# Optimization experiments

Measured on AMD Instinct MI355X. Metric: run time of the kernel, lower is better.

Reference implementation:

```python
import jax, jax.numpy as jnp
import numpy as np
from jax import lax

B, CIN, COUT, H, W = 8, 256, 256, 96, 96


def _conv_bn(x, w, g, b, act):
    # 3x3 conv, stride 1, SAME padding (NCHW / OIHW), then per-channel affine (folded BN)
    y = lax.conv_general_dilated(x, w, (1, 1), 'SAME',
                                 dimension_numbers=('NCHW', 'OIHW', 'NCHW'))
    y = y * g[None, :, None, None] + b[None, :, None, None]
    return jax.nn.relu(y) if act else y


def setup_inputs() -> dict:
    key = jax.random.key(0)
    ks = jax.random.split(key, 16)
    def wgt(k, cout, cin):
        return jax.random.normal(k, (cout, cin, 3, 3), jnp.float32) * (1.0 / np.sqrt(cin * 9))
    def gb(k, c):
        k1, k2 = jax.random.split(k)
        return (1.0 + 0.1 * jax.random.normal(k1, (c,), jnp.float32),
                0.1 * jax.random.normal(k2, (c,), jnp.float32))
    g_p1, b_p1 = gb(ks[1], COUT); g_p2, b_p2 = gb(ks[3], COUT)
    g_p, b_p = gb(ks[5], COUT); g_c1, b_c1 = gb(ks[7], COUT); g_c2, b_c2 = gb(ks[9], COUT)
    return {
        'x': jax.random.normal(ks[0], (B, CIN, H, W), jnp.float32),
        'w_p1': wgt(ks[10], COUT, CIN), 'g_p1': g_p1, 'b_p1': b_p1,
        'w_p2': wgt(ks[11], COUT, CIN), 'g_p2': g_p2, 'b_p2': b_p2,
        'w_p': wgt(ks[12], COUT, COUT), 'g_p': g_p, 'b_p': b_p,
        'w_c1': wgt(ks[13], COUT, CIN), 'g_c1': g_c1, 'b_c1': b_c1,
        'w_c2': wgt(ks[14], COUT, COUT), 'g_c2': g_c2, 'b_c2': b_c2,
    }


def reference(x, w_p1, g_p1, b_p1, w_p2, g_p2, b_p2, w_p, g_p, b_p,
              w_c1, g_c1, b_c1, w_c2, g_c2, b_c2):
    # branch 1: conv -> TopPool (cummax up, i.e. reverse along H) -> BottomPool (cummax down)
    p1 = _conv_bn(x, w_p1, g_p1, b_p1, act=True)
    pool1 = lax.cummax(p1, axis=2, reverse=True)   # TopPool
    pool1 = lax.cummax(pool1, axis=2)              # BottomPool
    # branch 2: conv -> LeftPool (reverse along W) -> RightPool
    p2 = _conv_bn(x, w_p2, g_p2, b_p2, act=True)
    pool2 = lax.cummax(p2, axis=3, reverse=True)   # LeftPool
    pool2 = lax.cummax(pool2, axis=3)              # RightPool
    p_conv = _conv_bn(pool1 + pool2, w_p, g_p, b_p, act=False)
    conv1 = _conv_bn(x, w_c1, g_c1, b_c1, act=False)
    relu = jax.nn.relu(p_conv + conv1)
    return _conv_bn(relu, w_c2, g_c2, b_c2, act=True)
```

## Files before the change

### kernel.cpp

```cpp
#include <hip/hip_runtime.h>


typedef _Float16 f16x8 __attribute__((ext_vector_type(8)));
typedef _Float16 f16x4v __attribute__((ext_vector_type(4)));
typedef float f32x4 __attribute__((ext_vector_type(4)));

#define HP 98
#define WP 98
#define KTOT 2304
#define WSET (256*KTOT)
#define XPAD_E ((size_t)8*HP*WP*256)
#define UVP_E  ((size_t)8*98*256)
#define UV2_E  ((size_t)3*8*96*256)
#define WUV_SET 196608

__device__ __forceinline__ int xcd_swz(int bid, int nwg)
{
  return (bid & 7) * (nwg >> 3) + (bid >> 3);
}

#define BUF_Q 24576
#define SMEM_Q 49152

struct CtxQ {
  unsigned goff[6];
  unsigned mask;
  unsigned lds_stage;
  unsigned aoff;
  int wl, quad, wv;
  int b, h0, w0;
};

template<int SW>
__device__ __forceinline__ CtxQ make_ctxQ(int spatial, int ch)
{
  CtxQ c;
  c.b = spatial / 36;
  const int tt = spatial - c.b * 36;
  const int ht = tt / 6, wt = tt - ht * 6;
  c.h0 = ht * 16; c.w0 = wt * 16;
  const int tid = threadIdx.x, lane = tid & 63;
  c.wv = tid >> 6;
  c.quad = lane >> 4; c.wl = lane & 15;
  c.aoff = (unsigned)((ch * 4 + c.wv * 2) * 512 + c.wl * 32 + c.quad * 8);
  const unsigned base_hw = (unsigned)(c.b * HP + c.h0) * WP + c.w0;
  const int lg = lane >> 2;
  c.mask = 0;
#pragma unroll
  for (int t = 0; t < 6; ++t) {
    const int s = (c.wv * 12 + t) * 16 + lg;
    const int x = s / 18, y = s - x * 18;
    const int wh = SW ? y : x, ww = SW ? x : y;
    c.goff[t] = (base_hw + (unsigned)(wh * WP + ww)) * 256u + (lane & 3) * 8u;
    if (y >= 12) c.mask |= (1u << t);
    if (s > 227) c.mask |= (1u << (6 + t));
  }
  c.lds_stage = (unsigned)(c.wv * 12) * 1024u + (unsigned)lane * 16u;
  return c;
}

template<int SW>
__device__ __forceinline__ void stage_cbQ(const _Float16* __restrict__ src,
                                          char* sbuf, const CtxQ& c, int buf, int cb)
{
  constexpr int D0 = SW ? (6 * WP + 5) * 256 : (5 * WP + 6) * 256;
  constexpr int D1 = SW ? (6 - 12 * WP) * 256 : (6 * WP - 12) * 256;
  char* l0 = sbuf + buf * BUF_Q + c.lds_stage;
#pragma unroll
  for (int t = 0; t < 6; ++t) {
    const _Float16* g = src + c.goff[t] + cb * 32;
    __builtin_amdgcn_global_load_lds(
        (const __attribute__((address_space(1))) void*)g,
        (__attribute__((address_space(3))) void*)(l0 + t * 1024), 16, 0, 0);
  }
#pragma unroll
  for (int t = 0; t < 6; ++t) {
    const int d = ((c.mask >> (6 + t)) & 1) ? 0
                : (((c.mask >> t) & 1) ? D1 : D0);
    const _Float16* g = src + (int)(c.goff[t] + (unsigned)d) + cb * 32;
    __builtin_amdgcn_global_load_lds(
        (const __attribute__((address_space(1))) void*)g,
        (__attribute__((address_space(3))) void*)(l0 + (6 + t) * 1024), 16, 0, 0);
  }
}

template<int S>
__device__ __forceinline__ void conv_accumQ(const _Float16* __restrict__ src,
                                            const _Float16* __restrict__ wkb,
                                            char* sbuf, const CtxQ& c, f32x4 acc[2][16])
{
  const _Float16* A0 = wkb + c.aoff;
  stage_cbQ<S>(src, sbuf, c, 0, 0);
#pragma unroll 1
  for (int cb = 0; cb < 8; ++cb) {
    __syncthreads();
    if (cb < 7) stage_cbQ<S>(src, sbuf, c, (cb + 1) & 1, cb + 1);
    const _Float16* B = (const _Float16*)(sbuf + (cb & 1) * BUF_Q);
    const _Float16* A = A0 + cb * (9 * 8192);
#pragma unroll
    for (int o = 0; o < 3; ++o) {
      f16x8 af[3][2];
#pragma unroll
      for (int p = 0; p < 3; ++p) {
        const int tap = (S == 0) ? p * 3 + o : o * 3 + p;
#pragma unroll
        for (int i = 0; i < 2; ++i)
          af[p][i] = *(const f16x8*)(A + tap * 8192 + i * 512);
      }
#pragma unroll
      for (int jh = 0; jh < 2; ++jh) {
        f16x8 cache[10];
#pragma unroll
        for (int r = 0; r < 10; ++r)
          cache[r] = *(const f16x8*)(B + ((jh * 8 + r) * 18 + c.wl + o) * 32 + c.quad * 8);
#pragma unroll
        for (int p = 0; p < 3; ++p)
#pragma unroll
          for (int i = 0; i < 2; ++i)
#pragma unroll
            for (int j = 0; j < 8; ++j)
              acc[i][jh * 8 + j] = __builtin_amdgcn_mfma_f32_16x16x32_f16(
                  af[p][i], cache[j + p], acc[i][jh * 8 + j], 0, 0, 0);
      }
    }
  }
  __syncthreads();
}

#define ZERO_ACCQ(acc) \
  _Pragma("unroll") for (int i = 0; i < 2; ++i) \
  _Pragma("unroll") for (int j = 0; j < 16; ++j) acc[i][j] = (f32x4){0.f,0.f,0.f,0.f};

__global__ __launch_bounds__(128, 2) void k_conv_p12(
    const _Float16* __restrict__ xpad, const _Float16* __restrict__ wk,
    const float* __restrict__ bias1, const float* __restrict__ bias2,
    float* __restrict__ u_pad, float* __restrict__ v_pad)
{
  __shared__ __align__(16) char smem[SMEM_Q];
  const int lin = xcd_swz(blockIdx.x, 2304);
  const int set = lin >= 1152;
  const int rem = lin - set * 1152;
  const int spatial = rem >> 2, ch = rem & 3;
  f32x4 acc[2][16];
  ZERO_ACCQ(acc)
  if (set == 0) {
    CtxQ c = make_ctxQ<0>(spatial, ch);
    conv_accumQ<0>(xpad, wk, smem, c, acc);
#pragma unroll
    for (int i = 0; i < 2; ++i) {
      const int co = (ch * 4 + c.wv * 2 + i) * 16 + c.quad * 4;
      const float4 bs = *(const float4*)(bias1 + co);
      float m0 = 0.f, m1 = 0.f, m2 = 0.f, m3 = 0.f;
#pragma unroll
      for (int j = 0; j < 16; ++j) {
        m0 = fmaxf(m0, acc[i][j][0] + bs.x);
        m1 = fmaxf(m1, acc[i][j][1] + bs.y);
        m2 = fmaxf(m2, acc[i][j][2] + bs.z);
        m3 = fmaxf(m3, acc[i][j][3] + bs.w);
      }
      unsigned* tgt = (unsigned*)(u_pad + ((size_t)c.b * 98 + (c.w0 + c.wl + 1)) * 256 + co);
      atomicMax(tgt + 0, __float_as_uint(m0));
      atomicMax(tgt + 1, __float_as_uint(m1));
      atomicMax(tgt + 2, __float_as_uint(m2));
      atomicMax(tgt + 3, __float_as_uint(m3));
    }
  } else {
    CtxQ c = make_ctxQ<1>(spatial, ch);
    conv_accumQ<1>(xpad, wk + WSET, smem, c, acc);
#pragma unroll
    for (int i = 0; i < 2; ++i) {
      const int co = (ch * 4 + c.wv * 2 + i) * 16 + c.quad * 4;
      const float4 bs = *(const float4*)(bias2 + co);
      float m0 = 0.f, m1 = 0.f, m2 = 0.f, m3 = 0.f;
#pragma unroll
      for (int j = 0; j < 16; ++j) {
        m0 = fmaxf(m0, acc[i][j][0] + bs.x);
        m1 = fmaxf(m1, acc[i][j][1] + bs.y);
        m2 = fmaxf(m2, acc[i][j][2] + bs.z);
        m3 = fmaxf(m3, acc[i][j][3] + bs.w);
      }
      unsigned* tgt = (unsigned*)(v_pad + ((size_t)c.b * 98 + (c.h0 + c.wl + 1)) * 256 + co);
      atomicMax(tgt + 0, __float_as_uint(m0));
      atomicMax(tgt + 1, __float_as_uint(m1));
      atomicMax(tgt + 2, __float_as_uint(m2));
      atomicMax(tgt + 3, __float_as_uint(m3));
    }
  }
}

__global__ __launch_bounds__(256, 2) void k_uv1d(
    const float* __restrict__ u_pad, const float* __restrict__ v_pad,
    const _Float16* __restrict__ wuv, float* __restrict__ u2, float* __restrict__ v2)
{
  const int id = blockIdx.x;
  const int py = blockIdx.y;
  const int b = id & 7, cs = (id >> 3) % 3, t = id / 24;
  const float* src = t ? v_pad : u_pad;
  float* dst = t ? v2 : u2;
  const _Float16* A0 = wuv + (size_t)(t * 3 + cs) * WUV_SET;
  const int lane = threadIdx.x & 63, wv = threadIdx.x >> 6;
  const int quad = lane >> 4, l16 = lane & 15;

  f32x4 acc[4][3];
#pragma unroll
  for (int i = 0; i < 4; ++i)
#pragma unroll
    for (int j = 0; j < 3; ++j) acc[i][j] = (f32x4){0.f, 0.f, 0.f, 0.f};

#pragma unroll 1
  for (int kb = 0; kb < 24; ++kb) {
    const int dw = kb >> 3, cb = kb & 7;
    f16x8 bf[3];
#pragma unroll
    for (int j = 0; j < 3; ++j) {
      const int pos = py * 48 + j * 16 + l16;
      const float* p = src + ((size_t)b * 98 + (pos + dw)) * 256 + cb * 32 + quad * 8;
      const float4 x0 = *(const float4*)p;
      const float4 x1 = *(const float4*)(p + 4);
      f16x8 v;
      v[0] = (_Float16)x0.x; v[1] = (_Float16)x0.y; v[2] = (_Float16)x0.z; v[3] = (_Float16)x0.w;
      v[4] = (_Float16)x1.x; v[5] = (_Float16)x1.y; v[6] = (_Float16)x1.z; v[7] = (_Float16)x1.w;
      bf[j] = v;
    }
    f16x8 af[4];
#pragma unroll
    for (int i = 0; i < 4; ++i)
      af[i] = *(const f16x8*)(A0 + (size_t)(kb * 16 + wv * 4 + i) * 512 + l16 * 32 + quad * 8);
#pragma unroll
    for (int i = 0; i < 4; ++i)
#pragma unroll
      for (int j = 0; j < 3; ++j)
        acc[i][j] = __builtin_amdgcn_mfma_f32_16x16x32_f16(af[i], bf[j], acc[i][j], 0, 0, 0);
  }
#pragma unroll
  for (int i = 0; i < 4; ++i)
#pragma unroll
    for (int j = 0; j < 3; ++j) {
      const int pos = py * 48 + j * 16 + l16;
      const int co = wv * 64 + i * 16 + quad * 4;
      *(f32x4*)(dst + ((size_t)(cs * 8 + b) * 96 + pos) * 256 + co) = acc[i][j];
    }
}

__global__ __launch_bounds__(128, 2) void k_conv_c1f(
    const _Float16* __restrict__ xpad, const _Float16* __restrict__ wkc1,
    const float* __restrict__ bias_p, const float* __restrict__ bias_c1,
    const float* __restrict__ u2, const float* __restrict__ v2,
    _Float16* __restrict__ rpad)
{
  __shared__ __align__(16) char smem[SMEM_Q];
  const int lin = xcd_swz(blockIdx.x, 1152);
  const int spatial = lin >> 2, ch = lin & 3;
  CtxQ c = make_ctxQ<0>(spatial, ch);
  f32x4 acc[2][16];
  ZERO_ACCQ(acc)
  conv_accumQ<0>(xpad, wkc1, smem, c, acc);

  const int w = c.w0 + c.wl;
  const int wcase = (w == 0) ? 0 : ((w == 95) ? 2 : 1);
#pragma unroll
  for (int i = 0; i < 2; ++i) {
    const int co = (ch * 4 + c.wv * 2 + i) * 16 + c.quad * 4;
    float4 bs = *(const float4*)(bias_p + co);
    const float4 b2 = *(const float4*)(bias_c1 + co);
    bs.x += b2.x; bs.y += b2.y; bs.z += b2.z; bs.w += b2.w;
#pragma unroll
    for (int j = 0; j < 16; ++j) {
      const int h = c.h0 + j;
      const int hcase = (h == 0) ? 0 : ((h == 95) ? 2 : 1);
      const float4 uq = *(const float4*)(u2 + ((size_t)(hcase * 8 + c.b) * 96 + w) * 256 + co);
      const float4 vq = *(const float4*)(v2 + ((size_t)(wcase * 8 + c.b) * 96 + h) * 256 + co);
      f16x4v pk;
      pk[0] = (_Float16)fmaxf(acc[i][j][0] + bs.x + uq.x + vq.x, 0.f);
      pk[1] = (_Float16)fmaxf(acc[i][j][1] + bs.y + uq.y + vq.y, 0.f);
      pk[2] = (_Float16)fmaxf(acc[i][j][2] + bs.z + uq.z + vq.z, 0.f);
      pk[3] = (_Float16)fmaxf(acc[i][j][3] + bs.w + uq.w + vq.w, 0.f);
      *(f16x4v*)(rpad + ((size_t)(c.b * HP + h + 1) * WP + w + 1) * 256 + co) = pk;
    }
  }
}

__global__ __launch_bounds__(128, 2) void k_conv_c2(
    const _Float16* __restrict__ rpad, const _Float16* __restrict__ wkc2,
    const float* __restrict__ bias, float* __restrict__ dout)
{
  __shared__ __align__(16) char smem[SMEM_Q];
  const int lin = xcd_swz(blockIdx.x, 1152);
  const int spatial = lin >> 2, ch = lin & 3;
  CtxQ c = make_ctxQ<0>(spatial, ch);
  f32x4 acc[2][16];
  ZERO_ACCQ(acc)
  conv_accumQ<0>(rpad, wkc2, smem, c, acc);

  const int w = c.w0 + c.wl;
#pragma unroll
  for (int j = 0; j < 16; ++j) {
    const int h = c.h0 + j;
    float* op = dout + (size_t)c.b * 2359296 + h * 96 + w;
#pragma unroll
    for (int i = 0; i < 2; ++i) {
      const int co = (ch * 4 + c.wv * 2 + i) * 16 + c.quad * 4;
      const float4 bs = *(const float4*)(bias + co);
      op[(size_t)(co + 0) * 9216] = fmaxf(acc[i][j][0] + bs.x, 0.f);
      op[(size_t)(co + 1) * 9216] = fmaxf(acc[i][j][1] + bs.y, 0.f);
      op[(size_t)(co + 2) * 9216] = fmaxf(acc[i][j][2] + bs.z, 0.f);
      op[(size_t)(co + 3) * 9216] = fmaxf(acc[i][j][3] + bs.w, 0.f);
    }
  }
}

__global__ void k_border(_Float16* __restrict__ xpad, _Float16* __restrict__ rpad)
{
  const int idx = blockIdx.x, b = blockIdx.y;
  _Float16* buf = blockIdx.z ? rpad : xpad;
  int h, w;
  if (idx < 98)       { h = 0;  w = idx; }
  else if (idx < 196) { h = 97; w = idx - 98; }
  else { const int r = idx - 196; h = 1 + (r >> 1); w = (r & 1) ? 97 : 0; }
  buf[((size_t)(b * HP + h) * WP + w) * 256 + threadIdx.x] = (_Float16)0.f;
}

__global__ void k_pack_x(const float* __restrict__ x, _Float16* __restrict__ xpad)
{
  __shared__ float tile[32][33];
  const int bh = blockIdx.x;
  const int b = bh / 96, h = bh - b * 96;
  const int c0 = blockIdx.y * 32, w0 = blockIdx.z * 32;
  const int tx = threadIdx.x & 31, ty = threadIdx.x >> 5;
#pragma unroll
  for (int i = 0; i < 4; ++i) {
    int cI = c0 + ty + i * 8;
    tile[ty + i * 8][tx] = x[(((size_t)b * 256 + cI) * 96 + h) * 96 + w0 + tx];
  }
  __syncthreads();
#pragma unroll
  for (int i = 0; i < 4; ++i) {
    int w = w0 + ty + i * 8;
    xpad[((size_t)(b * HP + h + 1) * WP + (w + 1)) * 256 + c0 + tx] =
        (_Float16)tile[tx][ty + i * 8];
  }
}

__global__ void k_repack_w(const float* w0, const float* g0, const float* w1, const float* g1,
                           const float* w2, const float* g2, const float* w3, const float* g3,
                           const float* w4, const float* g4, _Float16* __restrict__ wk)
{
  const int set = blockIdx.y;
  const float* w; const float* g;
  switch (set) {
    case 0: w = w0; g = g0; break;
    case 1: w = w1; g = g1; break;
    case 2: w = w2; g = g2; break;
    case 3: w = w3; g = g3; break;
    default: w = w4; g = g4; break;
  }
  const int t = blockIdx.x * 256 + threadIdx.x;
  const int co = t >> 8, ci = t & 255;
  const int cb = ci >> 5, kk = ci & 31, cog = co >> 4, m = co & 15;
  const float gv = g[co];
  const float* src = w + ((size_t)co * 256 + ci) * 9;
  _Float16* dst = wk + (size_t)set * WSET + cog * 512 + m * 32 + kk;
#pragma unroll
  for (int tap = 0; tap < 9; ++tap)
    dst[(cb * 9 + tap) * 8192] = (_Float16)(src[tap] * gv);
}

__global__ void k_repack_uvw(const float* __restrict__ wp, const float* __restrict__ gp,
                             _Float16* __restrict__ wuv)
{
  const int tcs = blockIdx.y;
  const int tt = tcs / 3, cs = tcs - tt * 3;
  const int idx = blockIdx.x * 256 + threadIdx.x;
  const int co = idx >> 8, ci = idx & 255;
  const float gv = gp[co];
  const float* src = wp + ((size_t)co * 256 + ci) * 9;
  const int lo = (cs == 0) ? 1 : 0, hi = (cs == 2) ? 1 : 2;
  _Float16* base = wuv + (size_t)tcs * WUV_SET;
#pragma unroll
  for (int d = 0; d < 3; ++d) {
    float s = 0.f;
    for (int e = lo; e <= hi; ++e)
      s += (tt == 0) ? src[e * 3 + d] : src[d * 3 + e];
    const int k = d * 256 + ci;
    const int kb = k >> 5, kk = k & 31;
    base[(size_t)(kb * 16 + (co >> 4)) * 512 + (co & 15) * 32 + kk] = (_Float16)(s * gv);
  }
}

extern "C" void kernel_launch(void* const* d_in, const int* in_sizes, int n_in,
                              void* d_out, int out_size, void* d_ws, size_t ws_size,
                              hipStream_t stream)
{
  const float* x    = (const float*)d_in[0];
  const float* w_p1 = (const float*)d_in[1];
  const float* g_p1 = (const float*)d_in[2];
  const float* b_p1 = (const float*)d_in[3];
  const float* w_p2 = (const float*)d_in[4];
  const float* g_p2 = (const float*)d_in[5];
  const float* b_p2 = (const float*)d_in[6];
  const float* w_p  = (const float*)d_in[7];
  const float* g_p  = (const float*)d_in[8];
  const float* b_p  = (const float*)d_in[9];
  const float* w_c1 = (const float*)d_in[10];
  const float* g_c1 = (const float*)d_in[11];
  const float* b_c1 = (const float*)d_in[12];
  const float* w_c2 = (const float*)d_in[13];
  const float* g_c2 = (const float*)d_in[14];
  const float* b_c2 = (const float*)d_in[15];

  char* ws = (char*)d_ws;
  size_t off = 0;
  _Float16* x_pad = (_Float16*)(ws + off); off += XPAD_E * 2;
  _Float16* r_pad = (_Float16*)(ws + off); off += XPAD_E * 2;
  _Float16* wks   = (_Float16*)(ws + off); off += (size_t)5 * WSET * 2;
  _Float16* wuv   = (_Float16*)(ws + off); off += (size_t)6 * WUV_SET * 2;
  float*    u_pad = (float*)(ws + off);    off += UVP_E * 4;
  float*    v_pad = (float*)(ws + off);    off += UVP_E * 4;
  float*    u2    = (float*)(ws + off);    off += UV2_E * 4;
  float*    v2    = (float*)(ws + off);    off += UV2_E * 4;
  (void)ws_size; (void)in_sizes; (void)n_in; (void)out_size;

  hipMemsetAsync(u_pad, 0, UVP_E * 4, stream);
  hipMemsetAsync(v_pad, 0, UVP_E * 4, stream);

  k_border    <<<dim3(388, 8, 2), 256, 0, stream>>>(x_pad, r_pad);
  k_pack_x    <<<dim3(768, 8, 3), 256, 0, stream>>>(x, x_pad);
  k_repack_w  <<<dim3(256, 5),    256, 0, stream>>>(w_p1, g_p1, w_p2, g_p2, w_p, g_p,
                                                    w_c1, g_c1, w_c2, g_c2, wks);
  k_repack_uvw<<<dim3(256, 6),    256, 0, stream>>>(w_p, g_p, wuv);
  k_conv_p12  <<<2304, 128, 0, stream>>>(x_pad, wks, b_p1, b_p2, u_pad, v_pad);
  k_uv1d      <<<dim3(48, 2), 256, 0, stream>>>(u_pad, v_pad, wuv, u2, v2);
  k_conv_c1f  <<<1152, 128, 0, stream>>>(x_pad, wks + (size_t)3 * WSET, b_p, b_c1,
                                         u2, v2, r_pad);
  k_conv_c2   <<<1152, 128, 0, stream>>>(r_pad, wks + (size_t)4 * WSET, b_c2,
                                         (float*)d_out);
}
```

Before: 549.9 us.

## Merge conv_c1 into the p1/p2 conv launch and split its epilogue out

The x-sourced c1 convolution moves into the same launch as the p1/p2 convolutions. Blocks grow to 256 threads (four waves, eight 16-channel groups per block), so each staged input tile is reused across twice as many output channels, and staging becomes one 6-load pass per wave. The c1 result is written as fp16 into the output buffer as scratch. A new elementwise kernel then adds u2/v2, applies relu and writes r_pad. This puts more work in one big launch and halves input staging per output channel, but adds an fp16 round trip for the intermediate and an extra kernel.

Result: faster. 522.0 us (-5.1%).

```diff
diff --git a/kernel.cpp b/kernel.cpp
--- a/kernel.cpp
+++ b/kernel.cpp
@@ -24,6 +24,99 @@
 
 struct CtxQ {
   unsigned goff[6];
+  unsigned lds_stage;
+  unsigned aoff;
+  int wl, quad, wv;
+  int b, h0, w0;
+};
+
+template<int SW>
+__device__ __forceinline__ CtxQ make_ctxQ(int spatial, int ch)
+{
+  CtxQ c;
+  c.b = spatial / 36;
+  const int tt = spatial - c.b * 36;
+  const int ht = tt / 6, wt = tt - ht * 6;
+  c.h0 = ht * 16; c.w0 = wt * 16;
+  const int tid = threadIdx.x, lane = tid & 63;
+  c.wv = tid >> 6;
+  c.quad = lane >> 4; c.wl = lane & 15;
+  c.aoff = (unsigned)((ch * 8 + c.wv * 2) * 512 + c.wl * 32 + c.quad * 8);
+  const unsigned base_hw = (unsigned)(c.b * HP + c.h0) * WP + c.w0;
+#pragma unroll
+  for (int t = 0; t < 6; ++t) {
+    int s = (c.wv * 6 + t) * 16 + (lane >> 2);
+    if (s > 323) s = 323;
+    const int x = s / 18, y = s - x * 18;
+    const int wh = SW ? y : x, ww = SW ? x : y;
+    c.goff[t] = (base_hw + (unsigned)(wh * WP + ww)) * 256u + (lane & 3) * 8u;
+  }
+  c.lds_stage = (unsigned)(c.wv * 6) * 1024u + (unsigned)lane * 16u;
+  return c;
+}
+
+__device__ __forceinline__ void stage_cbQ(const _Float16* __restrict__ src,
+                                          char* sbuf, const CtxQ& c, int buf, int cb)
+{
+  char* l0 = sbuf + buf * BUF_Q + c.lds_stage;
+#pragma unroll
+  for (int t = 0; t < 6; ++t) {
+    const _Float16* g = src + c.goff[t] + cb * 32;
+    __builtin_amdgcn_global_load_lds(
+        (const __attribute__((address_space(1))) void*)g,
+        (__attribute__((address_space(3))) void*)(l0 + t * 1024), 16, 0, 0);
+  }
+}
+
+template<int S>
+__device__ __forceinline__ void conv_accumQ(const _Float16* __restrict__ src,
+                                            const _Float16* __restrict__ wkb,
+                                            char* sbuf, const CtxQ& c, f32x4 acc[2][16])
+{
+  const _Float16* A0 = wkb + c.aoff;
+  stage_cbQ(src, sbuf, c, 0, 0);
+#pragma unroll 1
+  for (int cb = 0; cb < 8; ++cb) {
+    __syncthreads();
+    if (cb < 7) stage_cbQ(src, sbuf, c, (cb + 1) & 1, cb + 1);
+    const _Float16* B = (const _Float16*)(sbuf + (cb & 1) * BUF_Q);
+    const _Float16* A = A0 + cb * (9 * 8192);
+#pragma unroll
+    for (int o = 0; o < 3; ++o) {
+      f16x8 af[3][2];
+#pragma unroll
+      for (int p = 0; p < 3; ++p) {
+        const int tap = (S == 0) ? p * 3 + o : o * 3 + p;
+#pragma unroll
+        for (int i = 0; i < 2; ++i)
+          af[p][i] = *(const f16x8*)(A + tap * 8192 + i * 512);
+      }
+#pragma unroll
+      for (int jh = 0; jh < 2; ++jh) {
+        f16x8 cache[10];
+#pragma unroll
+        for (int r = 0; r < 10; ++r)
+          cache[r] = *(const f16x8*)(B + ((jh * 8 + r) * 18 + c.wl + o) * 32 + c.quad * 8);
+#pragma unroll
+        for (int p = 0; p < 3; ++p)
+#pragma unroll
+          for (int i = 0; i < 2; ++i)
+#pragma unroll
+            for (int j = 0; j < 8; ++j)
+              acc[i][jh * 8 + j] = __builtin_amdgcn_mfma_f32_16x16x32_f16(
+                  af[p][i], cache[j + p], acc[i][jh * 8 + j], 0, 0, 0);
+      }
+    }
+  }
+  __syncthreads();
+}
+
+#define ZERO_ACCQ(acc) \
+  _Pragma("unroll") for (int i = 0; i < 2; ++i) \
+  _Pragma("unroll") for (int j = 0; j < 16; ++j) acc[i][j] = (f32x4){0.f,0.f,0.f,0.f};
+
+struct CtxB {
+  unsigned goff[6];
   unsigned mask;
   unsigned lds_stage;
   unsigned aoff;
@@ -32,9 +125,9 @@
 };
 
 template<int SW>
-__device__ __forceinline__ CtxQ make_ctxQ(int spatial, int ch)
-{
-  CtxQ c;
+__device__ __forceinline__ CtxB make_ctxB(int spatial, int ch)
+{
+  CtxB c;
   c.b = spatial / 36;
   const int tt = spatial - c.b * 36;
   const int ht = tt / 6, wt = tt - ht * 6;
@@ -60,8 +153,8 @@
 }
 
 template<int SW>
-__device__ __forceinline__ void stage_cbQ(const _Float16* __restrict__ src,
-                                          char* sbuf, const CtxQ& c, int buf, int cb)
+__device__ __forceinline__ void stage_cbB(const _Float16* __restrict__ src,
+                                          char* sbuf, const CtxB& c, int buf, int cb)
 {
   constexpr int D0 = SW ? (6 * WP + 5) * 256 : (5 * WP + 6) * 256;
   constexpr int D1 = SW ? (6 - 12 * WP) * 256 : (6 * WP - 12) * 256;
@@ -85,16 +178,16 @@
 }
 
 template<int S>
-__device__ __forceinline__ void conv_accumQ(const _Float16* __restrict__ src,
+__device__ __forceinline__ void conv_accumB(const _Float16* __restrict__ src,
                                             const _Float16* __restrict__ wkb,
-                                            char* sbuf, const CtxQ& c, f32x4 acc[2][16])
+                                            char* sbuf, const CtxB& c, f32x4 acc[2][16])
 {
   const _Float16* A0 = wkb + c.aoff;
-  stage_cbQ<S>(src, sbuf, c, 0, 0);
+  stage_cbB<S>(src, sbuf, c, 0, 0);
 #pragma unroll 1
   for (int cb = 0; cb < 8; ++cb) {
     __syncthreads();
-    if (cb < 7) stage_cbQ<S>(src, sbuf, c, (cb + 1) & 1, cb + 1);
+    if (cb < 7) stage_cbB<S>(src, sbuf, c, (cb + 1) & 1, cb + 1);
     const _Float16* B = (const _Float16*)(sbuf + (cb & 1) * BUF_Q);
     const _Float16* A = A0 + cb * (9 * 8192);
 #pragma unroll
@@ -127,63 +220,86 @@
   __syncthreads();
 }
 
-#define ZERO_ACCQ(acc) \
-  _Pragma("unroll") for (int i = 0; i < 2; ++i) \
-  _Pragma("unroll") for (int j = 0; j < 16; ++j) acc[i][j] = (f32x4){0.f,0.f,0.f,0.f};
-
-__global__ __launch_bounds__(128, 2) void k_conv_p12(
+__global__ __launch_bounds__(256, 2) void k_conv_main(
     const _Float16* __restrict__ xpad, const _Float16* __restrict__ wk,
     const float* __restrict__ bias1, const float* __restrict__ bias2,
-    float* __restrict__ u_pad, float* __restrict__ v_pad)
+    const float* __restrict__ bias_p, const float* __restrict__ bias_c1,
+    float* __restrict__ u_pad, float* __restrict__ v_pad,
+    _Float16* __restrict__ tmp)
 {
   __shared__ __align__(16) char smem[SMEM_Q];
-  const int lin = xcd_swz(blockIdx.x, 2304);
-  const int set = lin >= 1152;
-  const int rem = lin - set * 1152;
-  const int spatial = rem >> 2, ch = rem & 3;
+  const int lin = xcd_swz(blockIdx.x, 1728);
   f32x4 acc[2][16];
   ZERO_ACCQ(acc)
-  if (set == 0) {
+  if (lin < 1152) {
+    const int set = lin >= 576;
+    const int rem = lin - set * 576;
+    const int spatial = rem >> 1, ch = rem & 1;
+    if (set == 0) {
+      CtxQ c = make_ctxQ<0>(spatial, ch);
+      conv_accumQ<0>(xpad, wk, smem, c, acc);
+#pragma unroll
+      for (int i = 0; i < 2; ++i) {
+        const int co = (ch * 8 + c.wv * 2 + i) * 16 + c.quad * 4;
+        const float4 bs = *(const float4*)(bias1 + co);
+        float m0 = 0.f, m1 = 0.f, m2 = 0.f, m3 = 0.f;
+#pragma unroll
+        for (int j = 0; j < 16; ++j) {
+          m0 = fmaxf(m0, acc[i][j][0] + bs.x);
+          m1 = fmaxf(m1, acc[i][j][1] + bs.y);
+          m2 = fmaxf(m2, acc[i][j][2] + bs.z);
+          m3 = fmaxf(m3, acc[i][j][3] + bs.w);
+        }
+        unsigned* tgt = (unsigned*)(u_pad + ((size_t)c.b * 98 + (c.w0 + c.wl + 1)) * 256 + co);
+        atomicMax(tgt + 0, __float_as_uint(m0));
+        atomicMax(tgt + 1, __float_as_uint(m1));
+        atomicMax(tgt + 2, __float_as_uint(m2));
+        atomicMax(tgt + 3, __float_as_uint(m3));
+      }
+    } else {
+      CtxQ c = make_ctxQ<1>(spatial, ch);
+      conv_accumQ<1>(xpad, wk + WSET, smem, c, acc);
+#pragma unroll
+      for (int i = 0; i < 2; ++i) {
+        const int co = (ch * 8 + c.wv * 2 + i) * 16 + c.quad * 4;
+        const float4 bs = *(const float4*)(bias2 + co);
+        float m0 = 0.f, m1 = 0.f, m2 = 0.f, m3 = 0.f;
+#pragma unroll
+        for (int j = 0; j < 16; ++j) {
+          m0 = fmaxf(m0, acc[i][j][0] + bs.x);
+          m1 = fmaxf(m1, acc[i][j][1] + bs.y);
+          m2 = fmaxf(m2, acc[i][j][2] + bs.z);
+          m3 = fmaxf(m3, acc[i][j][3] + bs.w);
+        }
+        unsigned* tgt = (unsigned*)(v_pad + ((size_t)c.b * 98 + (c.h0 + c.wl + 1)) * 256 + co);
+        atomicMax(tgt + 0, __float_as_uint(m0));
+        atomicMax(tgt + 1, __float_as_uint(m1));
+        atomicMax(tgt + 2, __float_as_uint(m2));
+        atomicMax(tgt + 3, __float_as_uint(m3));
+      }
+    }
+  } else {
+    const int idx = lin - 1152;
+    const int spatial = idx >> 1, ch = idx & 1;
     CtxQ c = make_ctxQ<0>(spatial, ch);
-    conv_accumQ<0>(xpad, wk, smem, c, acc);
+    conv_accumQ<0>(xpad, wk + (size_t)3 * WSET, smem, c, acc);
+    const int w = c.w0 + c.wl;
 #pragma unroll
     for (int i = 0; i < 2; ++i) {
-      const int co = (ch * 4 + c.wv * 2 + i) * 16 + c.quad * 4;
-      const float4 bs = *(const float4*)(bias1 + co);
-      float m0 = 0.f, m1 = 0.f, m2 = 0.f, m3 = 0.f;
+      const int co = (ch * 8 + c.wv * 2 + i) * 16 + c.quad * 4;
+      float4 bs = *(const float4*)(bias_p + co);
+      const float4 b2 = *(const float4*)(bias_c1 + co);
+      bs.x += b2.x; bs.y += b2.y; bs.z += b2.z; bs.w += b2.w;
 #pragma unroll
       for (int j = 0; j < 16; ++j) {
-        m0 = fmaxf(m0, acc[i][j][0] + bs.x);
-        m1 = fmaxf(m1, acc[i][j][1] + bs.y);
-        m2 = fmaxf(m2, acc[i][j][2] + bs.z);
-        m3 = fmaxf(m3, acc[i][j][3] + bs.w);
-      }
-      unsigned* tgt = (unsigned*)(u_pad + ((size_t)c.b * 98 + (c.w0 + c.wl + 1)) * 256 + co);
-      atomicMax(tgt + 0, __float_as_uint(m0));
-      atomicMax(tgt + 1, __float_as_uint(m1));
-      atomicMax(tgt + 2, __float_as_uint(m2));
-      atomicMax(tgt + 3, __float_as_uint(m3));
-    }
-  } else {
-    CtxQ c = make_ctxQ<1>(spatial, ch);
-    conv_accumQ<1>(xpad, wk + WSET, smem, c, acc);
-#pragma unroll
-    for (int i = 0; i < 2; ++i) {
-      const int co = (ch * 4 + c.wv * 2 + i) * 16 + c.quad * 4;
-      const float4 bs = *(const float4*)(bias2 + co);
-      float m0 = 0.f, m1 = 0.f, m2 = 0.f, m3 = 0.f;
-#pragma unroll
-      for (int j = 0; j < 16; ++j) {
-        m0 = fmaxf(m0, acc[i][j][0] + bs.x);
-        m1 = fmaxf(m1, acc[i][j][1] + bs.y);
-        m2 = fmaxf(m2, acc[i][j][2] + bs.z);
-        m3 = fmaxf(m3, acc[i][j][3] + bs.w);
-      }
-      unsigned* tgt = (unsigned*)(v_pad + ((size_t)c.b * 98 + (c.h0 + c.wl + 1)) * 256 + co);
-      atomicMax(tgt + 0, __float_as_uint(m0));
-      atomicMax(tgt + 1, __float_as_uint(m1));
-      atomicMax(tgt + 2, __float_as_uint(m2));
-      atomicMax(tgt + 3, __float_as_uint(m3));
+        const int h = c.h0 + j;
+        f16x4v pk;
+        pk[0] = (_Float16)(acc[i][j][0] + bs.x);
+        pk[1] = (_Float16)(acc[i][j][1] + bs.y);
+        pk[2] = (_Float16)(acc[i][j][2] + bs.z);
+        pk[3] = (_Float16)(acc[i][j][3] + bs.w);
+        *(f16x4v*)(tmp + ((size_t)(c.b * 96 + h) * 96 + w) * 256 + co) = pk;
+      }
     }
   }
 }
@@ -242,55 +358,50 @@
     }
 }
 
-__global__ __launch_bounds__(128, 2) void k_conv_c1f(
-    const _Float16* __restrict__ xpad, const _Float16* __restrict__ wkc1,
-    const float* __restrict__ bias_p, const float* __restrict__ bias_c1,
+__global__ __launch_bounds__(256, 8) void k_epi_c1(
+    const _Float16* __restrict__ tmp,
     const float* __restrict__ u2, const float* __restrict__ v2,
     _Float16* __restrict__ rpad)
+{
+  const int gid = blockIdx.x;
+  const int b = gid / 96, h = gid - b * 96;
+  const int hcase = (h == 0) ? 0 : ((h == 95) ? 2 : 1);
+  const size_t tbase = (size_t)(b * 96 + h) * 96 * 256;
+#pragma unroll 1
+  for (int it = 0; it < 12; ++it) {
+    const int chunk = it * 256 + threadIdx.x;
+    const int w = chunk >> 5;
+    const int co8 = (chunk & 31) * 8;
+    const int wcase = (w == 0) ? 0 : ((w == 95) ? 2 : 1);
+    const f16x8 t = *(const f16x8*)(tmp + tbase + (size_t)w * 256 + co8);
+    const float* up = u2 + ((size_t)(hcase * 8 + b) * 96 + w) * 256 + co8;
+    const float* vp = v2 + ((size_t)(wcase * 8 + b) * 96 + h) * 256 + co8;
+    const float4 u0 = *(const float4*)up, u1 = *(const float4*)(up + 4);
+    const float4 v0 = *(const float4*)vp, v1 = *(const float4*)(vp + 4);
+    f16x8 r;
+    r[0] = (_Float16)fmaxf((float)t[0] + u0.x + v0.x, 0.f);
+    r[1] = (_Float16)fmaxf((float)t[1] + u0.y + v0.y, 0.f);
+    r[2] = (_Float16)fmaxf((float)t[2] + u0.z + v0.z, 0.f);
+    r[3] = (_Float16)fmaxf((float)t[3] + u0.w + v0.w, 0.f);
+    r[4] = (_Float16)fmaxf((float)t[4] + u1.x + v1.x, 0.f);
+    r[5] = (_Float16)fmaxf((float)t[5] + u1.y + v1.y, 0.f);
+    r[6] = (_Float16)fmaxf((float)t[6] + u1.z + v1.z, 0.f);
+    r[7] = (_Float16)fmaxf((float)t[7] + u1.w + v1.w, 0.f);
+    *(f16x8*)(rpad + ((size_t)(b * HP + h + 1) * WP + w + 1) * 256 + co8) = r;
+  }
+}
+
+__global__ __launch_bounds__(128, 2) void k_conv_c2(
+    const _Float16* __restrict__ rpad, const _Float16* __restrict__ wkc2,
+    const float* __restrict__ bias, float* __restrict__ dout)
 {
   __shared__ __align__(16) char smem[SMEM_Q];
   const int lin = xcd_swz(blockIdx.x, 1152);
   const int spatial = lin >> 2, ch = lin & 3;
-  CtxQ c = make_ctxQ<0>(spatial, ch);
+  CtxB c = make_ctxB<0>(spatial, ch);
   f32x4 acc[2][16];
   ZERO_ACCQ(acc)
-  conv_accumQ<0>(xpad, wkc1, smem, c, acc);
-
-  const int w = c.w0 + c.wl;
-  const int wcase = (w == 0) ? 0 : ((w == 95) ? 2 : 1);
-#pragma unroll
-  for (int i = 0; i < 2; ++i) {
-    const int co = (ch * 4 + c.wv * 2 + i) * 16 + c.quad * 4;
-    float4 bs = *(const float4*)(bias_p + co);
-    const float4 b2 = *(const float4*)(bias_c1 + co);
-    bs.x += b2.x; bs.y += b2.y; bs.z += b2.z; bs.w += b2.w;
-#pragma unroll
-    for (int j = 0; j < 16; ++j) {
-      const int h = c.h0 + j;
-      const int hcase = (h == 0) ? 0 : ((h == 95) ? 2 : 1);
-      const float4 uq = *(const float4*)(u2 + ((size_t)(hcase * 8 + c.b) * 96 + w) * 256 + co);
-      const float4 vq = *(const float4*)(v2 + ((size_t)(wcase * 8 + c.b) * 96 + h) * 256 + co);
-      f16x4v pk;
-      pk[0] = (_Float16)fmaxf(acc[i][j][0] + bs.x + uq.x + vq.x, 0.f);
-      pk[1] = (_Float16)fmaxf(acc[i][j][1] + bs.y + uq.y + vq.y, 0.f);
-      pk[2] = (_Float16)fmaxf(acc[i][j][2] + bs.z + uq.z + vq.z, 0.f);
-      pk[3] = (_Float16)fmaxf(acc[i][j][3] + bs.w + uq.w + vq.w, 0.f);
-      *(f16x4v*)(rpad + ((size_t)(c.b * HP + h + 1) * WP + w + 1) * 256 + co) = pk;
-    }
-  }
-}
-
-__global__ __launch_bounds__(128, 2) void k_conv_c2(
-    const _Float16* __restrict__ rpad, const _Float16* __restrict__ wkc2,
-    const float* __restrict__ bias, float* __restrict__ dout)
-{
-  __shared__ __align__(16) char smem[SMEM_Q];
-  const int lin = xcd_swz(blockIdx.x, 1152);
-  const int spatial = lin >> 2, ch = lin & 3;
-  CtxQ c = make_ctxQ<0>(spatial, ch);
-  f32x4 acc[2][16];
-  ZERO_ACCQ(acc)
-  conv_accumQ<0>(rpad, wkc2, smem, c, acc);
+  conv_accumB<0>(rpad, wkc2, smem, c, acc);
 
   const int w = c.w0 + c.wl;
 #pragma unroll
@@ -418,6 +529,7 @@
   float*    v_pad = (float*)(ws + off);    off += UVP_E * 4;
   float*    u2    = (float*)(ws + off);    off += UV2_E * 4;
   float*    v2    = (float*)(ws + off);    off += UV2_E * 4;
+  _Float16* tmp   = (_Float16*)d_out;
   (void)ws_size; (void)in_sizes; (void)n_in; (void)out_size;
 
   hipMemsetAsync(u_pad, 0, UVP_E * 4, stream);
@@ -428,10 +540,10 @@
   k_repack_w  <<<dim3(256, 5),    256, 0, stream>>>(w_p1, g_p1, w_p2, g_p2, w_p, g_p,
                                                     w_c1, g_c1, w_c2, g_c2, wks);
   k_repack_uvw<<<dim3(256, 6),    256, 0, stream>>>(w_p, g_p, wuv);
-  k_conv_p12  <<<2304, 128, 0, stream>>>(x_pad, wks, b_p1, b_p2, u_pad, v_pad);
+  k_conv_main <<<1728, 256, 0, stream>>>(x_pad, wks, b_p1, b_p2, b_p, b_c1,
+                                         u_pad, v_pad, tmp);
   k_uv1d      <<<dim3(48, 2), 256, 0, stream>>>(u_pad, v_pad, wuv, u2, v2);
-  k_conv_c1f  <<<1152, 128, 0, stream>>>(x_pad, wks + (size_t)3 * WSET, b_p, b_c1,
-                                         u2, v2, r_pad);
+  k_epi_c1    <<<768, 256, 0, stream>>>(tmp, u2, v2, r_pad);
   k_conv_c2   <<<1152, 128, 0, stream>>>(r_pad, wks + (size_t)4 * WSET, b_c2,
                                          (float*)d_out);
 }
```
